# Performance work log

Hardware: AMD Instinct MI355X
Metric: run time of the kernel (lower is better)

Reference implementation:

```python
import jax, jax.numpy as jnp
import numpy as np

B, T, C = 1, 2048, 2048
H, N = 16, 128            # num_attention_heads, head_size
KVH = 4                   # num_key_value_heads
N_REP = H // KVH
D_DECAY, D_AAA, D_MV, D_MK, D_GATE = 160, 96, 64, 64, 160
ROPE_THETA = 1000000.0
EPS = 1e-6

def _rms_norm(h, w):
    var = jnp.mean(jnp.square(h.astype(jnp.float32)), axis=-1, keepdims=True)
    return (w * (h.astype(jnp.float32) * jax.lax.rsqrt(var + EPS))).astype(h.dtype)

def _rotate_half(q):
    q1, q2 = jnp.split(q, 2, axis=-1)
    return jnp.concatenate([-q2, q1], axis=-1)

def setup_inputs():
    key = jax.random.key(0)
    ks = jax.random.split(key, 24)
    f = jnp.float32
    rn = lambda k, shape, s=1.0: jax.random.normal(k, shape, dtype=f) * s
    half = N // 2
    inv_freq = 1.0 / (ROPE_THETA ** (jnp.arange(half, dtype=f) / half))
    freqs = jnp.arange(T, dtype=f)[:, None] * inv_freq[None, :]
    emb = jnp.concatenate([freqs, freqs], axis=-1)
    return {
        "x": rn(ks[0], (B, T, C)),
        "v_first": rn(ks[1], (B, T, KVH, N)),
        "k_first": rn(ks[2], (B, T, KVH, N)),
        "attention_mask": jnp.ones((B, T), f),
        "cos": jnp.cos(emb)[None],
        "sin": jnp.sin(emb)[None],
        "w0": rn(ks[3], (1, 1, H * N), 0.5) - 2.0,
        "w1": rn(ks[4], (C, D_DECAY), 0.02),
        "w2": rn(ks[5], (D_DECAY, H * N), 0.02),
        "a0": rn(ks[6], (1, 1, H * N), 0.1),
        "a1": rn(ks[7], (C, D_AAA), 0.02),
        "a2": rn(ks[8], (D_AAA, H * N), 0.02),
        "v0": rn(ks[9], (1, 1, KVH * N), 0.1) + 0.73,
        "v1": rn(ks[10], (C, D_MV), 0.02),
        "v2": rn(ks[11], (D_MV, KVH * N), 0.02),
        "k0": rn(ks[12], (1, 1, KVH * N), 0.1) + 0.73,
        "k1": rn(ks[13], (C, D_MK), 0.02),
        "k2": rn(ks[14], (D_MK, KVH * N), 0.02),
        "g1": rn(ks[15], (C, D_GATE), 0.02),
        "g2": rn(ks[16], (D_GATE, H * N), 0.02),
        "r_k": rn(ks[17], (H, N), 0.02) - 0.04,
        "r_norm_w": jnp.ones((N,), f),
        "k_norm_w": jnp.ones((N,), f),
        "W_r": rn(ks[18], (C, H * N), 0.02),
        "W_k": rn(ks[19], (C, KVH * N), 0.02),
        "W_v": rn(ks[20], (C, KVH * N), 0.02),
        "W_o": rn(ks[21], (H * N, C), 0.02),
    }

def _forward(x, v_first, k_first, attention_mask, cos, sin, w0, w1, w2, a0, a1, a2,
             v0, v1, v2, k0, k1, k2, g1, g2, r_k, r_norm_w, k_norm_w, W_r, W_k, W_v, W_o):
    xm = x * attention_mask[..., None]
    r = _rms_norm((xm @ W_r).reshape(B, T, H, N), r_norm_w)
    k = _rms_norm((xm @ W_k).reshape(B, T, KVH, N), k_norm_w)
    v = (xm @ W_v).reshape(B, T, KVH, N)
    c, s = cos[:, :, None, :], sin[:, :, None, :]   # rope, unsqueeze_dim=2
    r = r * c + _rotate_half(r) * s
    k = k * c + _rotate_half(k) * s
    w = -jax.nn.softplus(-(w0 + jnp.tanh(xm @ w1) @ w2)) - 0.5   # (B,T,H*N), always <= -0.5
    a = jax.nn.sigmoid(a0 + (xm @ a1) @ a2).reshape(B, T, H, N)  # in-context learning rate
    g = jax.nn.sigmoid(xm @ g1) @ g2                             # output gate (B,T,H*N)
    # residual mixing with first-layer value/key (layer_id > 0 branch)
    v = v + (v_first - v) * jax.nn.sigmoid(v0 + (xm @ v1) @ v2).reshape(B, T, KVH, N)
    k = k + (k_first - k) * jax.nn.sigmoid(k0 + (xm @ k1) @ k2).reshape(B, T, KVH, N)
    k = jnp.repeat(k, N_REP, axis=2)   # GQA repeat_kv -> (B,T,H,N)
    v = jnp.repeat(v, N_REP, axis=2)
    kk = k / jnp.maximum(jnp.linalg.norm(k, axis=-1, keepdims=True), 1e-12)  # F.normalize
    aa, bb = -kk, kk * a               # rank-1 state-update vectors
    wdec = jnp.exp(-jnp.exp(w.reshape(B, T, H, N)))  # per-channel decay in (0,1)

    def step(S, xs):                   # RWKV-7 state recurrence; S: (B,H,N,N) value x key
        wt, rt, kt, vt, at, bt = xs    # each (B,H,N)
        sa = jnp.einsum('bhij,bhj->bhi', S, at)
        S = S * wt[:, :, None, :] + sa[..., None] * bt[:, :, None, :] + vt[..., None] * kt[:, :, None, :]
        return S, jnp.einsum('bhij,bhj->bhi', S, rt)

    S0 = jnp.zeros((B, H, N, N), jnp.float32)
    xs = tuple(jnp.moveaxis(t, 1, 0) for t in (wdec, r, k, v, aa, bb))  # time-major
    _, y = jax.lax.scan(step, S0, xs)
    y = jnp.moveaxis(y, 0, 1)          # (B,T,H,N)
    y = y + jnp.sum(r * k * r_k, axis=-1, keepdims=True) * v   # r_k bonus term
    return (y.reshape(B, T, H * N) * g) @ W_o

def reference(x, v_first, k_first, attention_mask, cos, sin, w0, w1, w2, a0, a1, a2,
              v0, v1, v2, k0, k1, k2, g1, g2, r_k, r_norm_w, k_norm_w, W_r, W_k, W_v, W_o):
    return _forward(x, v_first, k_first, attention_mask, cos, sin, w0, w1, w2, a0, a1, a2,
                    v0, v1, v2, k0, k1, k2, g1, g2, r_k, r_norm_w, k_norm_w, W_r, W_k, W_v, W_o)
```

## Files before the change

kernel.cpp:

```cpp
#include <hip/hip_runtime.h>
#include <hip/hip_bf16.h>
#include <math.h>

#define T_   2048
#define C_   2048
#define H_   16
#define N_   128
#define KVH_ 4

typedef __bf16 bf16x8 __attribute__((ext_vector_type(8)));
typedef __bf16 bf16x4 __attribute__((ext_vector_type(4)));
typedef float  f32x4  __attribute__((ext_vector_type(4)));

#define MFMA16(a, b, c) __builtin_amdgcn_mfma_f32_16x16x32_bf16(a, b, c, 0, 0, 0)

static __device__ __forceinline__ void gll16(const __bf16* g, __bf16* l) {
    __builtin_amdgcn_global_load_lds((const __attribute__((address_space(1))) void*)g,
                                     (__attribute__((address_space(3))) void*)l, 16, 0, 0);
}

static __device__ __forceinline__ float wave_sum_shfl(float v) {
#pragma unroll
    for (int m = 32; m >= 1; m >>= 1) v += __shfl_xor(v, m, 64);
    return v;
}
static __device__ __forceinline__ float block_sum_128(float v, float* sh2) {
    v = wave_sum_shfl(v);
    if ((threadIdx.x & 63) == 0) sh2[threadIdx.x >> 6] = v;
    __syncthreads();
    float r = sh2[0] + sh2[1];
    __syncthreads();
    return r;
}

__global__ void xm_to_bf16(const float* __restrict__ x, const float* __restrict__ mask,
                           __bf16* __restrict__ o) {
    int idx = blockIdx.x * 256 + threadIdx.x;
    int e = idx * 4;
    float4 v = *(const float4*)(x + e);
    float m = mask[e >> 11];
    bf16x4 r;
    r.x = (__bf16)(v.x * m); r.y = (__bf16)(v.y * m);
    r.z = (__bf16)(v.z * m); r.w = (__bf16)(v.w * m);
    *(bf16x4*)(o + e) = r;
}

struct TrDesc { const float* src; __bf16* dst; int R, C, tileStart; };
struct TrBatch { TrDesc d[13]; int n; };

__global__ void transpose_batch(TrBatch tb) {
    int bid = blockIdx.x;
    int e = 0;
    while (e + 1 < tb.n && tb.d[e + 1].tileStart <= bid) e++;
    const float* src = tb.d[e].src;
    __bf16* dst = tb.d[e].dst;
    int R = tb.d[e].R, C = tb.d[e].C;
    int tix = bid - tb.d[e].tileStart;
    int tilesC = (C + 31) >> 5;
    int trow = tix / tilesC, tcol = tix - trow * tilesC;
    int r0 = trow * 32, c0 = tcol * 32;
    __shared__ float tile[32][33];
    int tx = threadIdx.x & 31, ty = threadIdx.x >> 5;
#pragma unroll
    for (int i = 0; i < 4; i++) {
        int r = r0 + ty + i * 8, c = c0 + tx;
        if (r < R && c < C) tile[ty + i * 8][tx] = src[(size_t)r * C + c];
    }
    __syncthreads();
#pragma unroll
    for (int i = 0; i < 4; i++) {
        int c = c0 + ty + i * 8, r = r0 + tx;
        if (c < C && r < R) dst[(size_t)c * R + r] = (__bf16)tile[tx][ty + i * 8];
    }
}

__global__ void transpose_f32_bf16(const float* __restrict__ src, __bf16* __restrict__ dst,
                                   int R, int C) {
    __shared__ float tile[32][33];
    int tx = threadIdx.x & 31, ty = threadIdx.x >> 5;
    int c0 = blockIdx.x * 32, r0 = blockIdx.y * 32;
#pragma unroll
    for (int i = 0; i < 4; i++) {
        int r = r0 + ty + i * 8, c = c0 + tx;
        if (r < R && c < C) tile[ty + i * 8][tx] = src[(size_t)r * C + c];
    }
    __syncthreads();
#pragma unroll
    for (int i = 0; i < 4; i++) {
        int c = c0 + ty + i * 8, r = r0 + tx;
        if (c < C && r < R) dst[(size_t)c * R + r] = (__bf16)tile[tx][ty + i * 8];
    }
}

template <int MODE>
__global__ __launch_bounds__(256, 2)
void gemm_bf16(const __bf16* __restrict__ A, int lda, const __bf16* __restrict__ BT,
               const float* __restrict__ bias, float* __restrict__ Cf,
               __bf16* __restrict__ Cb, int N, int K, int act) {
    __shared__ __align__(16) __bf16 As[128 * 32];
    __shared__ __align__(16) __bf16 Bs[128 * 32];
    const int tid = threadIdx.x;
    const int lane = tid & 63, wave = tid >> 6;
    const int bm = blockIdx.y * 128, bn = blockIdx.x * 128;
    const int wm = (wave >> 1) * 64, wn = (wave & 1) * 64;
    const int prow = lane >> 2, pk = (lane & 3) * 8;
    const __bf16* ApA = A + (size_t)(bm + wave * 32 + prow) * lda + pk;
    const __bf16* BpA = BT + (size_t)(bn + wave * 32 + prow) * K + pk;
    const bool bokA = (bn + wave * 32 + prow) < N;
    const bool bokB = (bn + wave * 32 + 16 + prow) < N;
    __bf16* AsD = As + wave * 1024;
    __bf16* BsD = Bs + wave * 1024;
    const int lm = lane & 15, lq = lane >> 4;
    f32x4 acc[4][4] = {};
    for (int k0 = 0; k0 < K; k0 += 32) {
        __syncthreads();
        gll16(ApA + k0, AsD);
        gll16(ApA + (size_t)16 * lda + k0, AsD + 512);
        if (bokA) gll16(BpA + k0, BsD);
        if (bokB) gll16(BpA + (size_t)16 * K + k0, BsD + 512);
        __syncthreads();
        bf16x8 af[4], bfr[4];
#pragma unroll
        for (int i = 0; i < 4; i++)
            af[i] = *(const bf16x8*)(As + (wm + i * 16 + lm) * 32 + lq * 8);
#pragma unroll
        for (int j = 0; j < 4; j++)
            bfr[j] = *(const bf16x8*)(Bs + (wn + j * 16 + lm) * 32 + lq * 8);
#pragma unroll
        for (int i = 0; i < 4; i++)
#pragma unroll
            for (int j = 0; j < 4; j++)
                acc[i][j] = MFMA16(af[i], bfr[j], acc[i][j]);
    }
#pragma unroll
    for (int j = 0; j < 4; j++) {
        int col = bn + wn + j * 16 + lm;
        if (col >= N) continue;
        float bv = (MODE == 0 && bias) ? bias[col] : 0.f;
#pragma unroll
        for (int i = 0; i < 4; i++) {
            int row0 = bm + wm + i * 16 + lq * 4;
#pragma unroll
            for (int rg = 0; rg < 4; rg++) {
                float v = acc[i][j][rg] + bv;
                int row = row0 + rg;
                if (MODE == 0) {
                    if (act == 1) v = tanhf(v);
                    else if (act == 2) v = 1.f / (1.f + __expf(-v));
                    Cf[(size_t)row * N + col] = v;
                } else {
                    if (col < 3072) {
                        Cf[(size_t)row * 3072 + col] = v;
                    } else {
                        float vv = v;
                        if (col < 3232) vv = tanhf(v);
                        else if (col >= 3456) vv = 1.f / (1.f + __expf(-v));
                        Cb[(size_t)row * 544 + (col - 3072)] = (__bf16)vv;
                    }
                }
            }
        }
    }
}

struct GSeg { const __bf16* BT; const float* bias; float* Cf; int aoff, K, N, act, bx0; };
struct GB5 { GSeg s[5]; };

__global__ __launch_bounds__(256, 2)
void gemm_group(const __bf16* __restrict__ Abase, GB5 gb) {
    __shared__ __align__(16) __bf16 As[128 * 32];
    __shared__ __align__(16) __bf16 Bs[128 * 32];
    int e = 0;
    while (e + 1 < 5 && gb.s[e + 1].bx0 <= (int)blockIdx.x) e++;
    const GSeg sg = gb.s[e];
    const int K = sg.K, N = sg.N;
    const __bf16* A = Abase + sg.aoff;
    const int tid = threadIdx.x;
    const int lane = tid & 63, wave = tid >> 6;
    const int bm = blockIdx.y * 128, bn = (blockIdx.x - sg.bx0) * 128;
    const int wm = (wave >> 1) * 64, wn = (wave & 1) * 64;
    const int prow = lane >> 2, pk = (lane & 3) * 8;
    const __bf16* ApA = A + (size_t)(bm + wave * 32 + prow) * 544 + pk;
    const __bf16* BpA = sg.BT + (size_t)(bn + wave * 32 + prow) * K + pk;
    __bf16* AsD = As + wave * 1024;
    __bf16* BsD = Bs + wave * 1024;
    const int lm = lane & 15, lq = lane >> 4;
    f32x4 acc[4][4] = {};
    for (int k0 = 0; k0 < K; k0 += 32) {
        __syncthreads();
        gll16(ApA + k0, AsD);
        gll16(ApA + (size_t)16 * 544 + k0, AsD + 512);
        gll16(BpA + k0, BsD);
        gll16(BpA + (size_t)16 * K + k0, BsD + 512);
        __syncthreads();
        bf16x8 af[4], bfr[4];
#pragma unroll
        for (int i = 0; i < 4; i++)
            af[i] = *(const bf16x8*)(As + (wm + i * 16 + lm) * 32 + lq * 8);
#pragma unroll
        for (int j = 0; j < 4; j++)
            bfr[j] = *(const bf16x8*)(Bs + (wn + j * 16 + lm) * 32 + lq * 8);
#pragma unroll
        for (int i = 0; i < 4; i++)
#pragma unroll
            for (int j = 0; j < 4; j++)
                acc[i][j] = MFMA16(af[i], bfr[j], acc[i][j]);
    }
#pragma unroll
    for (int j = 0; j < 4; j++) {
        int col = bn + wn + j * 16 + lm;
        float bv = sg.bias ? sg.bias[col] : 0.f;
#pragma unroll
        for (int i = 0; i < 4; i++) {
            int row0 = bm + wm + i * 16 + lq * 4;
#pragma unroll
            for (int rg = 0; rg < 4; rg++) {
                float v = acc[i][j][rg] + bv;
                if (sg.act == 2) v = 1.f / (1.f + __expf(-v));
                sg.Cf[(size_t)(row0 + rg) * N + col] = v;
            }
        }
    }
}

__global__ __launch_bounds__(128)
void prep_kv(float* __restrict__ mega, float* __restrict__ kkO,
             const float* __restrict__ kfirst, const float* __restrict__ vfirst,
             const float* __restrict__ kmix, const float* __restrict__ vmix,
             const float* __restrict__ cosT, const float* __restrict__ sinT,
             const float* __restrict__ knw) {
    __shared__ float sh[128];
    __shared__ float sh2[2];
    int b = blockIdx.x;
    int t = b >> 2, kvh = b & 3;
    int n = threadIdx.x;
    size_t kbase = (size_t)t * 3072 + 2048 + kvh * 128;
    size_t vbase = (size_t)t * 3072 + 2560 + kvh * 128;
    size_t fbase = (size_t)t * 512 + kvh * 128;
    float x = mega[kbase + n];
    float ssq = block_sum_128(x * x, sh2);
    float kn = knw[n] * (x * rsqrtf(ssq * (1.f / 128.f) + 1e-6f));
    sh[n] = kn;
    __syncthreads();
    float rot = (n < 64) ? -sh[n + 64] : sh[n - 64];
    float c = cosT[(size_t)t * 128 + n], s = sinT[(size_t)t * 128 + n];
    float kr = kn * c + rot * s;
    float kf = kr + (kfirst[fbase + n] - kr) * kmix[fbase + n];
    float s2 = block_sum_128(kf * kf, sh2);
    float kkv = kf / fmaxf(sqrtf(s2), 1e-12f);
    float vv = mega[vbase + n];
    float vf = vv + (vfirst[fbase + n] - vv) * vmix[fbase + n];
    mega[kbase + n] = kf;
    kkO[fbase + n] = kkv;
    mega[vbase + n] = vf;
}

__global__ __launch_bounds__(128)
void prep_r(float* __restrict__ mega, float* __restrict__ Wl,
            const float* __restrict__ rk, float* __restrict__ cOut,
            const float* __restrict__ cosT, const float* __restrict__ sinT,
            const float* __restrict__ rnw) {
    __shared__ float sh[128];
    __shared__ float sh2[2];
    int b = blockIdx.x;
    int t = b >> 4, h = b & 15;
    int kv = h >> 2;
    int n = threadIdx.x;
    size_t rbase = (size_t)t * 3072 + h * 128;
    float x = mega[rbase + n];
    float ssq = block_sum_128(x * x, sh2);
    float rn = rnw[n] * (x * rsqrtf(ssq * (1.f / 128.f) + 1e-6f));
    sh[n] = rn;
    __syncthreads();
    float rot = (n < 64) ? -sh[n + 64] : sh[n - 64];
    float c = cosT[(size_t)t * 128 + n], s = sinT[(size_t)t * 128 + n];
    float rr = rn * c + rot * s;
    mega[rbase + n] = rr;
    size_t wb_ = (size_t)t * 2048 + h * 128 + n;
    float z = Wl[wb_];
    float nz = -z;
    float sp = fmaxf(nz, 0.f) + log1pf(expf(-fabsf(nz)));
    float w = -sp - 0.5f;
    Wl[wb_] = expf(-expf(w));
    float pc = rr * mega[(size_t)t * 3072 + 2048 + kv * 128 + n] * rk[h * 128 + n];
    float cs = block_sum_128(pc, sh2);
    if (n == 0) cOut[b] = cs;
}


__global__ __launch_bounds__(64)
void scan_phaseA(const float* __restrict__ Wl, const float* __restrict__ megaF,
                 const float* __restrict__ aS, const float* __restrict__ kkB,
                 __bf16* __restrict__ ATt_g, __bf16* __restrict__ Rr_g,
                 __bf16* __restrict__ Bnt_g, __bf16* __restrict__ Knt_g,
                 __bf16* __restrict__ Vt_g, __bf16* __restrict__ Gbt_g,
                 __bf16* __restrict__ Gkt_g, float* __restrict__ Cloc_g,
                 float* __restrict__ cwL_g) {
    __shared__ __align__(16) __bf16 pool[27648];
    __bf16* Arm = pool;
    __bf16* Brm = pool + 4352;
    __bf16* Krm = pool + 8704;
    __bf16* Rrm = pool + 13056;
    __bf16* Vt  = pool + 17408;
    __bf16* Mrm = pool + 22528;
    __bf16* Mt  = pool + 23808;
    __bf16* Prm = pool + 25088;
    __bf16* Gtmp= pool + 26368;
    __bf16* M2rm = pool + 4352;
    __bf16* M2t  = pool + 5632;
    __bf16* Xa   = pool + 6912;
    __bf16* Xb   = pool + 8192;
    __bf16* Tt   = pool + 9472;
    __bf16* PTt  = pool + 10752;
    __bf16* Ant  = pool + 13056;

    const int l = threadIdx.x, lm = l & 15, lq = l >> 4;
    const int u = blockIdx.x, h = u >> 6, c = u & 63, kv = h >> 2;
    const int n0 = l, n1 = l + 64;

    float cw0 = 1.f, cw1 = 1.f;
    for (int t = 0; t < 32; ++t) {
        int tg = c * 32 + t;
        size_t hb = (size_t)tg * 2048 + h * 128;
        size_t mb = (size_t)tg * 3072;
        size_t kb = (size_t)tg * 512 + kv * 128;
        float wv0 = Wl[hb + n0], wv1 = Wl[hb + n1];
        float r0 = megaF[mb + h * 128 + n0], r1 = megaF[mb + h * 128 + n1];
        float q0 = kkB[kb + n0], q1 = kkB[kb + n1];
        float s0 = aS[hb + n0], s1 = aS[hb + n1];
        float k0 = megaF[mb + 2048 + kv * 128 + n0], k1 = megaF[mb + 2048 + kv * 128 + n1];
        float v0 = megaF[mb + 2560 + kv * 128 + n0], v1 = megaF[mb + 2560 + kv * 128 + n1];
        float cp0 = cw0, cp1 = cw1;
        cw0 *= wv0; cw1 *= wv1;
        float ic0 = 1.f / cw0, ic1 = 1.f / cw1;
        Arm[t * 136 + n0] = (__bf16)(-cp0 * q0);
        Arm[t * 136 + n1] = (__bf16)(-cp1 * q1);
        Brm[t * 136 + n0] = (__bf16)(q0 * s0 * ic0);
        Brm[t * 136 + n1] = (__bf16)(q1 * s1 * ic1);
        Krm[t * 136 + n0] = (__bf16)(k0 * ic0);
        Krm[t * 136 + n1] = (__bf16)(k1 * ic1);
        Rrm[t * 136 + n0] = (__bf16)(cw0 * r0);
        Rrm[t * 136 + n1] = (__bf16)(cw1 * r1);
        Vt[n0 * 40 + t] = (__bf16)v0;
        Vt[n1 * 40 + t] = (__bf16)v1;
    }
    cwL_g[(size_t)u * 128 + n0] = cw0;
    cwL_g[(size_t)u * 128 + n1] = cw1;
    __syncthreads();

    auto mmLL = [&](const __bf16* Ao, const __bf16* Bo, bool incl, __bf16* dTr, __bf16* dDir) {
#pragma unroll
        for (int ri = 0; ri < 2; ri++)
#pragma unroll
        for (int ci = 0; ci < 2; ci++) {
            f32x4 acc = {};
#pragma unroll
            for (int s = 0; s < 4; s++) {
                bf16x8 af = *(const bf16x8*)(Ao + (ri * 16 + lm) * 136 + s * 32 + lq * 8);
                bf16x8 bf = *(const bf16x8*)(Bo + (ci * 16 + lm) * 136 + s * 32 + lq * 8);
                acc = MFMA16(af, bf, acc);
            }
#pragma unroll
            for (int rg = 0; rg < 4; rg++) {
                int rr = ri * 16 + lq * 4 + rg, cc = ci * 16 + lm;
                bool keep = incl ? (cc <= rr) : (cc < rr);
                __bf16 bv = (__bf16)(keep ? acc[rg] : 0.f);
                if (dTr)  dTr[cc * 40 + rr] = bv;
                if (dDir) dDir[rr * 40 + cc] = bv;
            }
        }
    };
    mmLL(Arm, Brm, false, Mrm, Mt);
    mmLL(Arm, Krm, false, Prm, nullptr);
    mmLL(Rrm, Brm, true, nullptr, Gtmp);
    __syncthreads();
    for (int i = l; i < 512; i += 64) {
        int r = i >> 4, cp = i & 15;
        ((int*)(Gbt_g + (size_t)u * 1024))[i] = *(const int*)(Gtmp + r * 40 + cp * 2);
    }
    __syncthreads();
    mmLL(Rrm, Krm, true, nullptr, Gtmp);
    __syncthreads();
    for (int i = l; i < 512; i += 64) {
        int r = i >> 4, cp = i & 15;
        ((int*)(Gkt_g + (size_t)u * 1024))[i] = *(const int*)(Gtmp + r * 40 + cp * 2);
    }
    for (int i = l; i < 2048; i += 64) {
        int t = i >> 6, cp = i & 63;
        ((int*)(Rr_g + (size_t)u * 4096))[i] = *(const int*)(Rrm + t * 136 + cp * 2);
    }
    for (int i = l; i < 2048; i += 64) {
        int n = i >> 4, tp = i & 15;
        unsigned int lo = ((const unsigned short*)Brm)[(2 * tp) * 136 + n];
        unsigned int hi = ((const unsigned short*)Brm)[(2 * tp + 1) * 136 + n];
        ((unsigned int*)(Bnt_g + (size_t)u * 4096))[i] = lo | (hi << 16);
        unsigned int lo2 = ((const unsigned short*)Krm)[(2 * tp) * 136 + n];
        unsigned int hi2 = ((const unsigned short*)Krm)[(2 * tp + 1) * 136 + n];
        ((unsigned int*)(Knt_g + (size_t)u * 4096))[i] = lo2 | (hi2 << 16);
    }
    for (int i = l; i < 2048; i += 64) {
        int n = i >> 4, tp = i & 15;
        ((int*)(Vt_g + (size_t)u * 4096))[i] = *(const int*)(Vt + n * 40 + tp * 2);
    }
    __syncthreads();

    for (int i = l; i < 1024; i += 64) {
        int s = i >> 5, t = i & 31;
        Xa[s * 40 + t] = (s == t) ? (__bf16)1.f : Mrm[s * 40 + t];
    }
    for (int i = l; i < 4096; i += 64) {
        int s = i & 31, n = i >> 5;
        Ant[n * 32 + s] = Arm[s * 136 + n];
    }
    __syncthreads();

    auto mat32 = [&](const __bf16* Ao, const __bf16* Bo, const __bf16* accIn,
                     __bf16* oRm, __bf16* oT) {
#pragma unroll
        for (int ri = 0; ri < 2; ri++)
#pragma unroll
        for (int ci = 0; ci < 2; ci++) {
            f32x4 acc = {};
            if (accIn) {
#pragma unroll
                for (int rg = 0; rg < 4; rg++)
                    acc[rg] = (float)accIn[(ri * 16 + lq * 4 + rg) * 40 + ci * 16 + lm];
            }
            bf16x8 af = *(const bf16x8*)(Ao + (ri * 16 + lm) * 40 + lq * 8);
            bf16x8 bf = *(const bf16x8*)(Bo + (ci * 16 + lm) * 40 + lq * 8);
            acc = MFMA16(af, bf, acc);
#pragma unroll
            for (int rg = 0; rg < 4; rg++) {
                int rr = ri * 16 + lq * 4 + rg, cc = ci * 16 + lm;
                __bf16 bv = (__bf16)acc[rg];
                if (oRm) oRm[rr * 40 + cc] = bv;
                if (oT)  oT[cc * 40 + rr] = bv;
            }
        }
        __syncthreads();
    };
    mat32(Mrm, Mt, nullptr, M2rm, M2t);
    mat32(Xa, M2t, Xa, Xb, nullptr);
    mat32(M2rm, M2t, nullptr, Mrm, Mt);
    mat32(Xb, Mt, Xb, Xa, nullptr);
    mat32(Mrm, Mt, nullptr, M2rm, M2t);
    mat32(Xa, M2t, Xa, Xb, nullptr);
    mat32(M2rm, M2t, nullptr, Mrm, Mt);
    mat32(Xb, Mt, Xb, nullptr, Tt);
    mat32(Tt, Prm, nullptr, PTt, nullptr);

#pragma unroll
    for (int ti = 0; ti < 2; ti++) {
        bf16x8 af = *(const bf16x8*)(Tt + (ti * 16 + lm) * 40 + lq * 8);
#pragma unroll
        for (int ni = 0; ni < 8; ni++) {
            f32x4 accv = {};
            bf16x8 bfv = *(const bf16x8*)(Ant + (ni * 16 + lm) * 32 + lq * 8);
            accv = MFMA16(af, bfv, accv);
#pragma unroll
            for (int rg = 0; rg < 4; rg++)
                ATt_g[(size_t)u * 4096 + (ti * 16 + lq * 4 + rg) * 128 + ni * 16 + lm] = (__bf16)accv[rg];
        }
    }
#pragma unroll
    for (int ii = 0; ii < 8; ii++)
#pragma unroll
    for (int ti = 0; ti < 2; ti++) {
        f32x4 acc = {};
        bf16x8 af = *(const bf16x8*)(Vt + (ii * 16 + lm) * 40 + lq * 8);
        bf16x8 bf = *(const bf16x8*)(PTt + (ti * 16 + lm) * 40 + lq * 8);
        acc = MFMA16(af, bf, acc);
#pragma unroll
        for (int rg = 0; rg < 4; rg++)
            Cloc_g[(size_t)u * 4096 + (ii * 16 + lq * 4 + rg) * 32 + ti * 16 + lm] = acc[rg];
    }
}

struct OpsV {
    bf16x8 at[2], bn[2], kn[2], vf;
    f32x4 cl[2];
    float cw[2];
};

__global__ __launch_bounds__(256, 2)
void scan_phaseB(const __bf16* __restrict__ ATt_g, const __bf16* __restrict__ Bnt_g,
                 const __bf16* __restrict__ Knt_g, const __bf16* __restrict__ Vt_g,
                 const float* __restrict__ Cloc_g, const float* __restrict__ cwL_g,
                 __bf16* __restrict__ Sg, __bf16* __restrict__ Cg) {
    __shared__ __align__(16) __bf16 Ssl[4][16 * 40];
    __shared__ __align__(16) float Pl[2][4][16 * 36];
    const int h = blockIdx.y, i0 = blockIdx.x * 16;
    const int tid = threadIdx.x, w = tid >> 6, l = tid & 63;
    const int lm = l & 15, lq = l >> 4;
    f32x4 st[2] = {};

    auto loadOps = [&](int c, OpsV& o) {
        size_t u = (size_t)h * 64 + c;
#pragma unroll
        for (int j = 0; j < 2; j++) {
            o.at[j] = *(const bf16x8*)(ATt_g + u * 4096 + (size_t)(j * 16 + lm) * 128 + w * 32 + lq * 8);
            o.bn[j] = *(const bf16x8*)(Bnt_g + u * 4096 + (size_t)(w * 32 + j * 16 + lm) * 32 + lq * 8);
            o.kn[j] = *(const bf16x8*)(Knt_g + u * 4096 + (size_t)(w * 32 + j * 16 + lm) * 32 + lq * 8);
            o.cw[j] = cwL_g[u * 128 + w * 32 + j * 16 + lm];
        }
        o.vf = *(const bf16x8*)(Vt_g + u * 4096 + (size_t)(i0 + lm) * 32 + lq * 8);
        o.cl[0] = *(const f32x4*)(Cloc_g + u * 4096 + (size_t)(i0 + lm) * 32 + lq * 8);
        o.cl[1] = *(const f32x4*)(Cloc_g + u * 4096 + (size_t)(i0 + lm) * 32 + lq * 8 + 4);
    };

    auto compute = [&](int c, const OpsV& o) {
        size_t u = (size_t)h * 64 + c;
        int buf = c & 1;
#pragma unroll
        for (int j = 0; j < 2; j++)
#pragma unroll
            for (int rg = 0; rg < 4; rg++)
                Ssl[w][(lq * 4 + rg) * 40 + j * 16 + lm] = (__bf16)st[j][rg];
        bf16x8 saf = *(const bf16x8*)(&Ssl[w][lm * 40 + lq * 8]);
        f32x4 zz = {};
        f32x4 pc0 = MFMA16(saf, o.at[0], zz);
        f32x4 pc1 = MFMA16(saf, o.at[1], zz);
        *(bf16x8*)(Sg + u * 16384 + (size_t)(i0 + lm) * 128 + w * 32 + lq * 8) = saf;
#pragma unroll
        for (int rg = 0; rg < 4; rg++) {
            Pl[buf][w][(lq * 4 + rg) * 36 + lm] = pc0[rg];
            Pl[buf][w][(lq * 4 + rg) * 36 + 16 + lm] = pc1[rg];
        }
        __syncthreads();
        f32x4 s0 = o.cl[0], s1 = o.cl[1];
#pragma unroll
        for (int ww = 0; ww < 4; ww++) {
            s0 += *(const f32x4*)(&Pl[buf][ww][lm * 36 + lq * 8]);
            s1 += *(const f32x4*)(&Pl[buf][ww][lm * 36 + lq * 8 + 4]);
        }
        bf16x8 cf;
#pragma unroll
        for (int j = 0; j < 4; j++) { cf[j] = (__bf16)s0[j]; cf[4 + j] = (__bf16)s1[j]; }
        if (w == 0)
            *(bf16x8*)(Cg + u * 4096 + (size_t)(i0 + lm) * 32 + lq * 8) = cf;
#pragma unroll
        for (int j = 0; j < 2; j++) {
            f32x4 t = MFMA16(o.vf, o.kn[j], st[j]);
            t = MFMA16(cf, o.bn[j], t);
            float cwv = o.cw[j];
#pragma unroll
            for (int rg = 0; rg < 4; rg++) st[j][rg] = t[rg] * cwv;
        }
    };

    OpsV A, B;
    loadOps(0, A);
    loadOps(1, B);
    for (int c = 0; c < 64; c += 2) {
        compute(c, A);
        if (c + 2 < 64) loadOps(c + 2, A);
        compute(c + 1, B);
        if (c + 3 < 64) loadOps(c + 3, B);
    }
}

__global__ __launch_bounds__(64)
void scan_phaseC(const __bf16* __restrict__ Sg, const __bf16* __restrict__ Cg,
                 const __bf16* __restrict__ Rr_g, const __bf16* __restrict__ Vt_g,
                 const __bf16* __restrict__ Gbt_g, const __bf16* __restrict__ Gkt_g,
                 const float* __restrict__ cB, const float* __restrict__ megaF,
                 const float* __restrict__ gB, __bf16* __restrict__ out) {
    __shared__ float Ybuf[32 * 18];
    const int bx = blockIdx.x, h = blockIdx.y;
    const int c = bx >> 3, i0 = (bx & 7) * 16;
    const int l = threadIdx.x, lm = l & 15, lq = l >> 4;
    const size_t u = (size_t)h * 64 + c;
    bf16x8 saf[4];
#pragma unroll
    for (int s = 0; s < 4; s++)
        saf[s] = *(const bf16x8*)(Sg + u * 16384 + (size_t)(i0 + lm) * 128 + s * 32 + lq * 8);
    bf16x8 cf = *(const bf16x8*)(Cg + u * 4096 + (size_t)(i0 + lm) * 32 + lq * 8);
    bf16x8 vf = *(const bf16x8*)(Vt_g + u * 4096 + (size_t)(i0 + lm) * 32 + lq * 8);
#pragma unroll
    for (int ti = 0; ti < 2; ti++) {
        f32x4 acc = {};
#pragma unroll
        for (int s = 0; s < 4; s++) {
            bf16x8 rp = *(const bf16x8*)(Rr_g + u * 4096 + (ti * 16 + lm) * 128 + s * 32 + lq * 8);
            acc = MFMA16(saf[s], rp, acc);
        }
        bf16x8 gb = *(const bf16x8*)(Gbt_g + u * 1024 + (ti * 16 + lm) * 32 + lq * 8);
        acc = MFMA16(cf, gb, acc);
        bf16x8 gk = *(const bf16x8*)(Gkt_g + u * 1024 + (ti * 16 + lm) * 32 + lq * 8);
        acc = MFMA16(vf, gk, acc);
#pragma unroll
        for (int rg = 0; rg < 4; rg++)
            Ybuf[(ti * 16 + lm) * 18 + lq * 4 + rg] = acc[rg];
    }
    __syncthreads();
    const int kv = h >> 2;
#pragma unroll
    for (int pass = 0; pass < 8; pass++) {
        int t = pass * 4 + lq;
        int tg = c * 32 + t;
        int col = h * 128 + i0 + lm;
        float yv = Ybuf[t * 18 + lm];
        float cv = cB[tg * 16 + h];
        float vv = megaF[(size_t)tg * 3072 + 2560 + kv * 128 + i0 + lm];
        float gg = gB[(size_t)tg * 2048 + col];
        out[(size_t)tg * 2048 + col] = (__bf16)((yv + cv * vv) * gg);
    }
}

extern "C" void kernel_launch(void* const* d_in, const int* in_sizes, int n_in,
                              void* d_out, int out_size, void* d_ws, size_t ws_size,
                              hipStream_t stream) {
    (void)in_sizes; (void)n_in; (void)out_size; (void)ws_size;
    const float* x      = (const float*)d_in[0];
    const float* vfirst = (const float*)d_in[1];
    const float* kfirst = (const float*)d_in[2];
    const float* amask  = (const float*)d_in[3];
    const float* cosT   = (const float*)d_in[4];
    const float* sinT   = (const float*)d_in[5];
    const float* w0     = (const float*)d_in[6];
    const float* w1     = (const float*)d_in[7];
    const float* w2     = (const float*)d_in[8];
    const float* a0     = (const float*)d_in[9];
    const float* a1     = (const float*)d_in[10];
    const float* a2     = (const float*)d_in[11];
    const float* v0     = (const float*)d_in[12];
    const float* v1     = (const float*)d_in[13];
    const float* v2     = (const float*)d_in[14];
    const float* k0     = (const float*)d_in[15];
    const float* k1     = (const float*)d_in[16];
    const float* k2     = (const float*)d_in[17];
    const float* g1     = (const float*)d_in[18];
    const float* g2     = (const float*)d_in[19];
    const float* rk     = (const float*)d_in[20];
    const float* rnw    = (const float*)d_in[21];
    const float* knw    = (const float*)d_in[22];
    const float* W_r    = (const float*)d_in[23];
    const float* W_k    = (const float*)d_in[24];
    const float* W_v    = (const float*)d_in[25];
    const float* W_o    = (const float*)d_in[26];

    char* p = (char*)d_ws;
    auto take = [&](size_t bytes) { char* r = p; p += (bytes + 255) & ~(size_t)255; return r; };
    __bf16* arena   = (__bf16*)take((size_t)3616 * 2048 * 2);
    __bf16* xmb     = (__bf16*)take((size_t)T_ * C_ * 2);
    float*  megaF   = (float*)take((size_t)T_ * 3072 * 4);
    __bf16* megaB   = (__bf16*)take((size_t)T_ * 544 * 2);
    __bf16* w2T     = (__bf16*)take((size_t)2048 * 160 * 2);
    __bf16* a2T     = (__bf16*)take((size_t)2048 * 96 * 2);
    __bf16* v2T     = (__bf16*)take((size_t)512 * 64 * 2);
    __bf16* k2T     = (__bf16*)take((size_t)512 * 64 * 2);
    __bf16* g2T     = (__bf16*)take((size_t)2048 * 160 * 2);
    float*  Wl      = (float*)take((size_t)T_ * 2048 * 4);
    float*  aS      = (float*)take((size_t)T_ * 2048 * 4);
    float*  gB      = (float*)take((size_t)T_ * 2048 * 4);
    float*  kkB     = (float*)take((size_t)T_ * 512 * 4);
    float*  vmx     = (float*)take((size_t)T_ * 512 * 4);
    float*  kmx     = (float*)take((size_t)T_ * 512 * 4);
    float*  cB      = (float*)take((size_t)T_ * H_ * 4);
    __bf16* ATt_g   = (__bf16*)take((size_t)1024 * 4096 * 2);
    __bf16* Rr_g    = (__bf16*)take((size_t)1024 * 4096 * 2);
    __bf16* Bnt_g   = (__bf16*)take((size_t)1024 * 4096 * 2);
    __bf16* Knt_g   = (__bf16*)take((size_t)1024 * 4096 * 2);
    __bf16* Vt_g    = (__bf16*)take((size_t)1024 * 4096 * 2);
    __bf16* Gbt_g   = (__bf16*)take((size_t)1024 * 1024 * 2);
    __bf16* Gkt_g   = (__bf16*)take((size_t)1024 * 1024 * 2);
    float*  Cloc_g  = (float*)take((size_t)1024 * 4096 * 4);
    float*  cwL_g   = (float*)take((size_t)1024 * 128 * 4);
    __bf16* Sg = (__bf16*)Wl;
    __bf16* Cg = (__bf16*)kkB;

    xm_to_bf16<<<(T_ * C_ / 4) / 256, 256, 0, stream>>>(x, amask, xmb);

    TrBatch tb;
    {
        const float* srcs[13] = {W_r, W_k, W_v, w1, a1, v1, k1, g1, w2, a2, v2, k2, g2};
        __bf16* dsts[13] = {arena, arena + (size_t)2048 * 2048, arena + (size_t)2560 * 2048,
                            arena + (size_t)3072 * 2048, arena + (size_t)3232 * 2048,
                            arena + (size_t)3328 * 2048, arena + (size_t)3392 * 2048,
                            arena + (size_t)3456 * 2048, w2T, a2T, v2T, k2T, g2T};
        int Rs[13] = {2048, 2048, 2048, 2048, 2048, 2048, 2048, 2048, 160, 96, 64, 64, 160};
        int Cs[13] = {2048, 512, 512, 160, 96, 64, 64, 160, 2048, 2048, 512, 512, 2048};
        int cum = 0;
        for (int e = 0; e < 13; e++) {
            tb.d[e].src = srcs[e]; tb.d[e].dst = dsts[e];
            tb.d[e].R = Rs[e]; tb.d[e].C = Cs[e]; tb.d[e].tileStart = cum;
            cum += ((Rs[e] + 31) / 32) * ((Cs[e] + 31) / 32);
        }
        tb.n = 13;
        transpose_batch<<<cum, 256, 0, stream>>>(tb);
    }

    gemm_bf16<2><<<dim3(29, 16), 256, 0, stream>>>(xmb, 2048, arena, nullptr, megaF, megaB, 3616, 2048, 0);

    GB5 gb;
    gb.s[0] = {w2T, w0, Wl,  0,   160, 2048, 0, 0};
    gb.s[1] = {a2T, a0, aS,  160, 96,  2048, 2, 16};
    gb.s[2] = {v2T, v0, vmx, 256, 64,  512,  2, 32};
    gb.s[3] = {k2T, k0, kmx, 320, 64,  512,  2, 36};
    gb.s[4] = {g2T, nullptr, gB, 384, 160, 2048, 0, 40};
    gemm_group<<<dim3(56, 16), 256, 0, stream>>>(megaB, gb);

    prep_kv<<<T_ * KVH_, 128, 0, stream>>>(megaF, kkB, kfirst, vfirst, kmx, vmx, cosT, sinT, knw);
    prep_r<<<T_ * H_, 128, 0, stream>>>(megaF, Wl, rk, cB, cosT, sinT, rnw);

    scan_phaseA<<<1024, 64, 0, stream>>>(Wl, megaF, aS, kkB, ATt_g, Rr_g, Bnt_g, Knt_g,
                                         Vt_g, Gbt_g, Gkt_g, Cloc_g, cwL_g);
    scan_phaseB<<<dim3(8, 16), 256, 0, stream>>>(ATt_g, Bnt_g, Knt_g, Vt_g, Cloc_g, cwL_g, Sg, Cg);
    scan_phaseC<<<dim3(512, 16), 64, 0, stream>>>(Sg, Cg, Rr_g, Vt_g, Gbt_g, Gkt_g,
                                                  cB, megaF, gB, xmb);

    transpose_f32_bf16<<<dim3(64, 64), 256, 0, stream>>>(W_o, arena, 2048, 2048);
    gemm_bf16<0><<<dim3(16, 16), 256, 0, stream>>>(xmb, 2048, arena, nullptr, (float*)d_out, nullptr, 2048, 2048, 0);
}
```

Measured before the change: 503.5 us.

## Run scan phase B with one wave per block and drop single-wave barriers

Phase B of the chunked scan changes from four waves, each holding a 32-column slice of the state and reducing partial products through LDS with a block barrier, to a single wave. That wave holds the full 16x128 state slice in registers and does the whole chunk contraction itself with no cross-wave reduction. The __syncthreads calls in the 64-thread phase A and phase C kernels are also removed, since each of those blocks is one wave. The aim is to remove barrier and LDS-reduction overhead on the serial chunk recurrence. In exchange, each wave does four times the MFMA work per chunk, register pressure rises sharply (8 state accumulators plus large double-buffered operands), and correctness now relies on implicit wave-level ordering of LDS accesses.

```diff
diff --git a/kernel.cpp b/kernel.cpp
--- a/kernel.cpp
+++ b/kernel.cpp
@@ -346,7 +346,6 @@
     }
     cwL_g[(size_t)u * 128 + n0] = cw0;
     cwL_g[(size_t)u * 128 + n1] = cw1;
-    __syncthreads();
 
     auto mmLL = [&](const __bf16* Ao, const __bf16* Bo, bool incl, __bf16* dTr, __bf16* dDir) {
 #pragma unroll
@@ -373,14 +372,11 @@
     mmLL(Arm, Brm, false, Mrm, Mt);
     mmLL(Arm, Krm, false, Prm, nullptr);
     mmLL(Rrm, Brm, true, nullptr, Gtmp);
-    __syncthreads();
     for (int i = l; i < 512; i += 64) {
         int r = i >> 4, cp = i & 15;
         ((int*)(Gbt_g + (size_t)u * 1024))[i] = *(const int*)(Gtmp + r * 40 + cp * 2);
     }
-    __syncthreads();
     mmLL(Rrm, Krm, true, nullptr, Gtmp);
-    __syncthreads();
     for (int i = l; i < 512; i += 64) {
         int r = i >> 4, cp = i & 15;
         ((int*)(Gkt_g + (size_t)u * 1024))[i] = *(const int*)(Gtmp + r * 40 + cp * 2);
@@ -402,7 +398,6 @@
         int n = i >> 4, tp = i & 15;
         ((int*)(Vt_g + (size_t)u * 4096))[i] = *(const int*)(Vt + n * 40 + tp * 2);
     }
-    __syncthreads();
 
     for (int i = l; i < 1024; i += 64) {
         int s = i >> 5, t = i & 31;
@@ -412,7 +407,6 @@
         int s = i & 31, n = i >> 5;
         Ant[n * 32 + s] = Arm[s * 136 + n];
     }
-    __syncthreads();
 
     auto mat32 = [&](const __bf16* Ao, const __bf16* Bo, const __bf16* accIn,
                      __bf16* oRm, __bf16* oT) {
@@ -437,7 +431,6 @@
                 if (oT)  oT[cc * 40 + rr] = bv;
             }
         }
-        __syncthreads();
     };
     mat32(Mrm, Mt, nullptr, M2rm, M2t);
     mat32(Xa, M2t, Xa, Xb, nullptr);
@@ -476,85 +469,95 @@
     }
 }
 
-struct OpsV {
-    bf16x8 at[2], bn[2], kn[2], vf;
+struct Ops {
+    bf16x8 at[8], bn[8], kn[8], vf;
     f32x4 cl[2];
-    float cw[2];
+    float cw[8];
 };
 
-__global__ __launch_bounds__(256, 2)
+__global__ __launch_bounds__(64, 1)
 void scan_phaseB(const __bf16* __restrict__ ATt_g, const __bf16* __restrict__ Bnt_g,
                  const __bf16* __restrict__ Knt_g, const __bf16* __restrict__ Vt_g,
                  const float* __restrict__ Cloc_g, const float* __restrict__ cwL_g,
                  __bf16* __restrict__ Sg, __bf16* __restrict__ Cg) {
-    __shared__ __align__(16) __bf16 Ssl[4][16 * 40];
-    __shared__ __align__(16) float Pl[2][4][16 * 36];
+    __shared__ __align__(16) __bf16 Sbf[16 * 136];
+    __shared__ __align__(16) __bf16 Cbf[16 * 40];
     const int h = blockIdx.y, i0 = blockIdx.x * 16;
-    const int tid = threadIdx.x, w = tid >> 6, l = tid & 63;
-    const int lm = l & 15, lq = l >> 4;
-    f32x4 st[2] = {};
-
-    auto loadOps = [&](int c, OpsV& o) {
+    const int l = threadIdx.x, lm = l & 15, lq = l >> 4;
+    f32x4 st[8];
+#pragma unroll
+    for (int cc = 0; cc < 8; cc++) st[cc] = (f32x4){0.f, 0.f, 0.f, 0.f};
+
+    auto loadOps = [&](int c, Ops& o) {
         size_t u = (size_t)h * 64 + c;
-#pragma unroll
-        for (int j = 0; j < 2; j++) {
-            o.at[j] = *(const bf16x8*)(ATt_g + u * 4096 + (size_t)(j * 16 + lm) * 128 + w * 32 + lq * 8);
-            o.bn[j] = *(const bf16x8*)(Bnt_g + u * 4096 + (size_t)(w * 32 + j * 16 + lm) * 32 + lq * 8);
-            o.kn[j] = *(const bf16x8*)(Knt_g + u * 4096 + (size_t)(w * 32 + j * 16 + lm) * 32 + lq * 8);
-            o.cw[j] = cwL_g[u * 128 + w * 32 + j * 16 + lm];
+        const __bf16* ATp = ATt_g + u * 4096;
+        const __bf16* Bp  = Bnt_g + u * 4096;
+        const __bf16* Kp  = Knt_g + u * 4096;
+#pragma unroll
+        for (int ti = 0; ti < 2; ti++)
+#pragma unroll
+            for (int s = 0; s < 4; s++)
+                o.at[ti * 4 + s] = *(const bf16x8*)(ATp + (ti * 16 + lm) * 128 + s * 32 + lq * 8);
+#pragma unroll
+        for (int cc = 0; cc < 8; cc++) {
+            o.bn[cc] = *(const bf16x8*)(Bp + (cc * 16 + lm) * 32 + lq * 8);
+            o.kn[cc] = *(const bf16x8*)(Kp + (cc * 16 + lm) * 32 + lq * 8);
         }
         o.vf = *(const bf16x8*)(Vt_g + u * 4096 + (size_t)(i0 + lm) * 32 + lq * 8);
-        o.cl[0] = *(const f32x4*)(Cloc_g + u * 4096 + (size_t)(i0 + lm) * 32 + lq * 8);
-        o.cl[1] = *(const f32x4*)(Cloc_g + u * 4096 + (size_t)(i0 + lm) * 32 + lq * 8 + 4);
+#pragma unroll
+        for (int ti = 0; ti < 2; ti++)
+#pragma unroll
+            for (int rg = 0; rg < 4; rg++)
+                o.cl[ti][rg] = Cloc_g[u * 4096 + (i0 + lq * 4 + rg) * 32 + ti * 16 + lm];
+#pragma unroll
+        for (int cc = 0; cc < 8; cc++) o.cw[cc] = cwL_g[u * 128 + cc * 16 + lm];
     };
 
-    auto compute = [&](int c, const OpsV& o) {
+    auto computeChunk = [&](int c, const Ops& o) {
         size_t u = (size_t)h * 64 + c;
-        int buf = c & 1;
-#pragma unroll
-        for (int j = 0; j < 2; j++)
+#pragma unroll
+        for (int cc = 0; cc < 8; cc++)
 #pragma unroll
             for (int rg = 0; rg < 4; rg++)
-                Ssl[w][(lq * 4 + rg) * 40 + j * 16 + lm] = (__bf16)st[j][rg];
-        bf16x8 saf = *(const bf16x8*)(&Ssl[w][lm * 40 + lq * 8]);
-        f32x4 zz = {};
-        f32x4 pc0 = MFMA16(saf, o.at[0], zz);
-        f32x4 pc1 = MFMA16(saf, o.at[1], zz);
-        *(bf16x8*)(Sg + u * 16384 + (size_t)(i0 + lm) * 128 + w * 32 + lq * 8) = saf;
-#pragma unroll
-        for (int rg = 0; rg < 4; rg++) {
-            Pl[buf][w][(lq * 4 + rg) * 36 + lm] = pc0[rg];
-            Pl[buf][w][(lq * 4 + rg) * 36 + 16 + lm] = pc1[rg];
-        }
-        __syncthreads();
-        f32x4 s0 = o.cl[0], s1 = o.cl[1];
-#pragma unroll
-        for (int ww = 0; ww < 4; ww++) {
-            s0 += *(const f32x4*)(&Pl[buf][ww][lm * 36 + lq * 8]);
-            s1 += *(const f32x4*)(&Pl[buf][ww][lm * 36 + lq * 8 + 4]);
-        }
-        bf16x8 cf;
-#pragma unroll
-        for (int j = 0; j < 4; j++) { cf[j] = (__bf16)s0[j]; cf[4 + j] = (__bf16)s1[j]; }
-        if (w == 0)
-            *(bf16x8*)(Cg + u * 4096 + (size_t)(i0 + lm) * 32 + lq * 8) = cf;
-#pragma unroll
-        for (int j = 0; j < 2; j++) {
-            f32x4 t = MFMA16(o.vf, o.kn[j], st[j]);
-            t = MFMA16(cf, o.bn[j], t);
-            float cwv = o.cw[j];
-#pragma unroll
-            for (int rg = 0; rg < 4; rg++) st[j][rg] = t[rg] * cwv;
+                Sbf[(lq * 4 + rg) * 136 + cc * 16 + lm] = (__bf16)st[cc][rg];
+        bf16x8 saf[4];
+#pragma unroll
+        for (int s = 0; s < 4; s++)
+            saf[s] = *(const bf16x8*)(Sbf + lm * 136 + s * 32 + lq * 8);
+        f32x4 cacc[2];
+#pragma unroll
+        for (int ti = 0; ti < 2; ti++) {
+            f32x4 acc = o.cl[ti];
+#pragma unroll
+            for (int s = 0; s < 4; s++) acc = MFMA16(saf[s], o.at[ti * 4 + s], acc);
+            cacc[ti] = acc;
+        }
+#pragma unroll
+        for (int ti = 0; ti < 2; ti++)
+#pragma unroll
+            for (int rg = 0; rg < 4; rg++)
+                Cbf[(lq * 4 + rg) * 40 + ti * 16 + lm] = (__bf16)cacc[ti][rg];
+        bf16x8 cf = *(const bf16x8*)(Cbf + lm * 40 + lq * 8);
+#pragma unroll
+        for (int s = 0; s < 4; s++)
+            *(bf16x8*)(Sg + u * 16384 + (size_t)(i0 + lm) * 128 + s * 32 + lq * 8) = saf[s];
+        *(bf16x8*)(Cg + u * 4096 + (size_t)(i0 + lm) * 32 + lq * 8) = cf;
+#pragma unroll
+        for (int cc = 0; cc < 8; cc++) {
+            st[cc] = MFMA16(cf, o.bn[cc], st[cc]);
+            st[cc] = MFMA16(o.vf, o.kn[cc], st[cc]);
+#pragma unroll
+            for (int rg = 0; rg < 4; rg++) st[cc][rg] *= o.cw[cc];
         }
     };
 
-    OpsV A, B;
+    Ops A, B;
     loadOps(0, A);
     loadOps(1, B);
     for (int c = 0; c < 64; c += 2) {
-        compute(c, A);
+        computeChunk(c, A);
         if (c + 2 < 64) loadOps(c + 2, A);
-        compute(c + 1, B);
+        computeChunk(c + 1, B);
         if (c + 3 < 64) loadOps(c + 3, B);
     }
 }
@@ -592,7 +595,6 @@
         for (int rg = 0; rg < 4; rg++)
             Ybuf[(ti * 16 + lm) * 18 + lq * 4 + rg] = acc[rg];
     }
-    __syncthreads();
     const int kv = h >> 2;
 #pragma unroll
     for (int pass = 0; pass < 8; pass++) {
@@ -705,7 +707,7 @@
 
     scan_phaseA<<<1024, 64, 0, stream>>>(Wl, megaF, aS, kkB, ATt_g, Rr_g, Bnt_g, Knt_g,
                                          Vt_g, Gbt_g, Gkt_g, Cloc_g, cwL_g);
-    scan_phaseB<<<dim3(8, 16), 256, 0, stream>>>(ATt_g, Bnt_g, Knt_g, Vt_g, Cloc_g, cwL_g, Sg, Cg);
+    scan_phaseB<<<dim3(8, 16), 64, 0, stream>>>(ATt_g, Bnt_g, Knt_g, Vt_g, Cloc_g, cwL_g, Sg, Cg);
     scan_phaseC<<<dim3(512, 16), 64, 0, stream>>>(Sg, Cg, Rr_g, Vt_g, Gbt_g, Gkt_g,
                                                   cB, megaF, gB, xmb);
 
```

Result: slower. 519.0 us (+3.1%).
